# Kernel optimization log

Measured on AMD Instinct MI355X. Metric: run time of the kernel, lower is better.

The kernel has to match this reference:

```python
import jax, jax.numpy as jnp
import numpy as np

D_MODEL, N_HEADS, D_FFN = 256, 8, 1024
HEAD_DIM = D_MODEL // N_HEADS
BZ, H, W = 2, 56, 56
EPS = 1e-5


def _layer_norm(x, g, b):
    m = jnp.mean(x, axis=-1, keepdims=True)
    v = jnp.mean((x - m) ** 2, axis=-1, keepdims=True)
    return (x - m) / jnp.sqrt(v + EPS) * g + b


def _forward(src, posemb_row, posemb_col,
             w_q_row, b_q_row, w_q_col, b_q_col,
             w_k_row, b_k_row, w_k_col, b_k_col,
             w_v, b_v, w_out, b_out,
             norm1_g, norm1_b, lin1_w, lin1_b, lin2_w, lin2_b,
             norm2_g, norm2_b, padding_mask):
    bz, c, h, w = src.shape
    nq = h * w
    x = src.transpose(0, 2, 3, 1)                      # (b,h,w,c)
    x_pr = x + posemb_row[:, None, :, :]               # row posemb broadcast over h
    x_pc = x + posemb_col[:, :, None, :]               # col posemb broadcast over w
    scaling = HEAD_DIM ** -0.5

    q_row = (x_pr.reshape(bz, nq, c) @ w_q_row.T + b_q_row) * scaling
    q_col = (x_pc.reshape(bz, nq, c) @ w_q_col.T + b_q_col) * scaling
    k_row = (x_pr @ w_k_row.T + b_k_row).mean(axis=1)  # (b,w,c): pool over rows
    k_col = (x_pc @ w_k_col.T + b_k_col).mean(axis=2)  # (b,h,c): pool over cols
    v = x @ w_v.T + b_v                                # (b,h,w,c)

    q_row = q_row.reshape(bz, nq, N_HEADS, HEAD_DIM)
    q_col = q_col.reshape(bz, nq, N_HEADS, HEAD_DIM)
    k_row = k_row.reshape(bz, w, N_HEADS, HEAD_DIM)
    k_col = k_col.reshape(bz, h, N_HEADS, HEAD_DIM)
    v = v.reshape(bz, h, w, N_HEADS, HEAD_DIM)

    aw_row = jnp.einsum('bqnd,bwnd->bnqw', q_row, k_row)
    aw_col = jnp.einsum('bqnd,bhnd->bnqh', q_col, k_col)
    neg = jnp.finfo(aw_row.dtype).min
    aw_row = jnp.where(padding_mask[:, 0, :][:, None, None, :], neg, aw_row)
    aw_col = jnp.where(padding_mask[:, :, 0][:, None, None, :], neg, aw_col)
    aw_row = jax.nn.softmax(aw_row, axis=-1)
    aw_col = jax.nn.softmax(aw_col, axis=-1)

    # out[q] = sum_h A_col[q,h] * (sum_w A_row[q,w] * V[h,w])  (RCDA recombination)
    tmp = jnp.einsum('bnqw,bhwnd->bnqhd', aw_row, v)   # dominant intermediate
    attn = jnp.einsum('bnqh,bnqhd->bqnd', aw_col, tmp).reshape(bz, nq, c)
    attn = attn @ w_out.T + b_out                      # (b,hw,c)

    x = _layer_norm(x + attn.reshape(bz, h, w, c), norm1_g, norm1_b)
    y = jax.nn.relu(x @ lin1_w.T + lin1_b) @ lin2_w.T + lin2_b
    x = _layer_norm(x + y, norm2_g, norm2_b)
    return x.transpose(0, 3, 1, 2)                     # (b,c,h,w)


def setup_inputs() -> dict:
    key = jax.random.key(0)
    ks = jax.random.split(key, 12)

    def wmat(k, shape, scale=0.02):
        return jax.random.normal(k, shape, jnp.float32) * scale

    return {
        'src': jax.random.normal(ks[0], (BZ, D_MODEL, H, W), jnp.float32),
        'padding_mask': jnp.zeros((BZ, H, W), jnp.bool_),
        'posemb_row': jax.random.normal(ks[1], (BZ, W, D_MODEL), jnp.float32),
        'posemb_col': jax.random.normal(ks[2], (BZ, H, D_MODEL), jnp.float32),
        'w_q_row': wmat(ks[3], (D_MODEL, D_MODEL)),
        'b_q_row': jnp.zeros((D_MODEL,), jnp.float32),
        'w_q_col': wmat(ks[4], (D_MODEL, D_MODEL)),
        'b_q_col': jnp.zeros((D_MODEL,), jnp.float32),
        'w_k_row': wmat(ks[5], (D_MODEL, D_MODEL)),
        'b_k_row': jnp.zeros((D_MODEL,), jnp.float32),
        'w_k_col': wmat(ks[6], (D_MODEL, D_MODEL)),
        'b_k_col': jnp.zeros((D_MODEL,), jnp.float32),
        'w_v': wmat(ks[7], (D_MODEL, D_MODEL)),
        'b_v': jnp.zeros((D_MODEL,), jnp.float32),
        'w_out': wmat(ks[8], (D_MODEL, D_MODEL)),
        'b_out': jnp.zeros((D_MODEL,), jnp.float32),
        'norm1_g': jnp.ones((D_MODEL,), jnp.float32),
        'norm1_b': jnp.zeros((D_MODEL,), jnp.float32),
        'lin1_w': wmat(ks[9], (D_FFN, D_MODEL)),
        'lin1_b': jnp.zeros((D_FFN,), jnp.float32),
        'lin2_w': wmat(ks[10], (D_MODEL, D_FFN)),
        'lin2_b': jnp.zeros((D_MODEL,), jnp.float32),
        'norm2_g': jnp.ones((D_MODEL,), jnp.float32),
        'norm2_b': jnp.zeros((D_MODEL,), jnp.float32),
    }


def reference(src, padding_mask, posemb_row, posemb_col,
              w_q_row, b_q_row, w_q_col, b_q_col,
              w_k_row, b_k_row, w_k_col, b_k_col,
              w_v, b_v, w_out, b_out,
              norm1_g, norm1_b, lin1_w, lin1_b, lin2_w, lin2_b,
              norm2_g, norm2_b):
    return _forward(src, posemb_row, posemb_col,
                    w_q_row, b_q_row, w_q_col, b_q_col,
                    w_k_row, b_k_row, w_k_col, b_k_col,
                    w_v, b_v, w_out, b_out,
                    norm1_g, norm1_b, lin1_w, lin1_b, lin2_w, lin2_b,
                    norm2_g, norm2_b, padding_mask)
```

## Files before the change

### kernel.cpp

```cpp
#include <hip/hip_runtime.h>
#include <math.h>

#define EPSV 1e-5f
#define SCALV 0.17677669529663687f

typedef __attribute__((ext_vector_type(8))) short s16x8;
typedef __attribute__((ext_vector_type(8))) __bf16 bf8_t;
typedef __attribute__((ext_vector_type(4))) float f32x4;

__device__ inline unsigned short f2bfu(float f) {
  union { float f; unsigned u; } v; v.f = f;
  return (unsigned short)((v.u + 0x7FFFu + ((v.u >> 16) & 1u)) >> 16);
}

__device__ inline f32x4 mfma16(s16x8 a, s16x8 b, f32x4 c) {
  return __builtin_amdgcn_mfma_f32_16x16x32_bf16(
      __builtin_bit_cast(bf8_t, a), __builtin_bit_cast(bf8_t, b), c, 0, 0, 0);
}

__device__ inline void gll16(const void* g, const void* l) {
  __builtin_amdgcn_global_load_lds(
      (const __attribute__((address_space(1))) unsigned*)g,
      (__attribute__((address_space(3))) unsigned*)l, 16, 0, 0);
}

__global__ __launch_bounds__(256) void k_transpose(const float* __restrict__ src,
                                                   float* __restrict__ X,
                                                   short* __restrict__ Xb) {
  __shared__ float tile[32][33];
  int b = blockIdx.z;
  int hw0 = blockIdx.x * 32, c0 = blockIdx.y * 32;
  int tx = threadIdx.x, ty = threadIdx.y;
  for (int i = ty; i < 32; i += 8)
    tile[i][tx] = src[((size_t)(b * 256 + c0 + i)) * 3136 + hw0 + tx];
  __syncthreads();
  for (int i = ty; i < 32; i += 8) {
    float v = tile[tx][i];
    size_t idx = ((size_t)(b * 3136 + hw0 + i)) * 256 + c0 + tx;
    X[idx] = v;
    Xb[idx] = (short)f2bfu(v);
  }
}

__global__ void k_means(const float* __restrict__ src, float* __restrict__ MH, float* __restrict__ MW) {
  int c = blockIdx.x, b = blockIdx.y, t = threadIdx.x;
  if (t >= 56) return;
  const float* p = src + ((size_t)(b * 256 + c)) * 3136;
  float sH = 0.f, sW = 0.f;
  for (int i = 0; i < 56; ++i) {
    sH += p[i * 56 + t];
    sW += p[t * 56 + i];
  }
  MH[((size_t)(b * 56 + t)) * 256 + c] = sH * (1.f / 56.f);
  MW[((size_t)(b * 56 + t)) * 256 + c] = sW * (1.f / 56.f);
}

__global__ __launch_bounds__(256) void k_smallproj(
    const float* __restrict__ per, const float* __restrict__ pec,
    const float* __restrict__ mh, const float* __restrict__ mw,
    const float* __restrict__ wqr, const float* __restrict__ wqc,
    const float* __restrict__ wkr, const float* __restrict__ wkc,
    const float* __restrict__ bkr, const float* __restrict__ bkc,
    float* __restrict__ PRW, float* __restrict__ PCW,
    float* __restrict__ KR, float* __restrict__ KC) {
  __shared__ __align__(16) float inb[256];
  int s = blockIdx.x / 112;
  int r = blockIdx.x % 112;
  int j = threadIdx.x;
  const float* i0; const float* i1 = nullptr; const float* W;
  const float* bias = nullptr; float* out;
  if (s == 0)      { i0 = per; W = wqr; out = PRW; }
  else if (s == 1) { i0 = pec; W = wqc; out = PCW; }
  else if (s == 2) { i0 = per; i1 = mh; W = wkr; bias = bkr; out = KR; }
  else             { i0 = pec; i1 = mw; W = wkc; bias = bkc; out = KC; }
  float v = i0[(size_t)r * 256 + j];
  if (i1) v += i1[(size_t)r * 256 + j];
  inb[j] = v;
  __syncthreads();
  const float* wrow = W + (size_t)j * 256;
  float acc = 0.f;
  #pragma unroll
  for (int c4 = 0; c4 < 64; ++c4) {
    float4 iv = *(const float4*)(&inb[c4 * 4]);
    float4 wv = *(const float4*)(wrow + c4 * 4);
    acc += iv.x * wv.x + iv.y * wv.y + iv.z * wv.z + iv.w * wv.w;
  }
  if (bias) acc += bias[j];
  out[(size_t)r * 256 + j] = acc;
}

__global__ __launch_bounds__(256) void k_pack(
    const float* __restrict__ wqr, const float* __restrict__ wqc, const float* __restrict__ wv,
    const float* __restrict__ wo, const float* __restrict__ l1w, const float* __restrict__ l2w,
    short* __restrict__ Wcat, short* __restrict__ wob,
    short* __restrict__ l1b, short* __restrict__ l2b) {
  int seg = blockIdx.y;
  int e = (blockIdx.x * 256 + threadIdx.x) * 4;
  int cnt = (seg == 0) ? 196608 : (seg == 1) ? 65536 : 262144;
  if (e >= cnt) return;
  const float* sp;
  short* dp;
  if (seg == 0) {
    dp = Wcat + e;
    sp = (e < 65536) ? wqr + e : (e < 131072) ? wqc + (e - 65536) : wv + (e - 131072);
  } else if (seg == 1) { dp = wob + e; sp = wo + e; }
  else if (seg == 2)   { dp = l1b + e; sp = l1w + e; }
  else                 { dp = l2b + e; sp = l2w + e; }
  float4 v = *(const float4*)sp;
  uint2 p;
  p.x = (unsigned)f2bfu(v.x) | ((unsigned)f2bfu(v.y) << 16);
  p.y = (unsigned)f2bfu(v.z) | ((unsigned)f2bfu(v.w) << 16);
  *(uint2*)dp = p;
}

#define GEMM64_CORE(Aptr, Wptr, Kdim)                                           \
  __shared__ __align__(16) short Ls[2][2][4096];                                \
  int tid = threadIdx.x;                                                        \
  int wid = tid >> 6, lane = tid & 63;                                          \
  int ln15 = lane & 15, slot = lane >> 4;                                       \
  int m0 = blockIdx.x * 64, n0 = blockIdx.y * 64;                               \
  int l8 = lane >> 3, c8 = lane & 7;                                            \
  int csw = ((c8 ^ l8) << 4);                                                   \
  int K2 = (Kdim) * 2;                                                          \
  const char* Ag = (const char*)(Aptr) + (size_t)(m0 + wid * 16 + l8) * K2 + csw; \
  const char* Wg = (const char*)(Wptr) + (size_t)(n0 + wid * 16 + l8) * K2 + csw; \
  int u0 = __builtin_amdgcn_readfirstlane(wid * 2048);                          \
  int wm0 = (wid >> 1) << 5, wn0 = (wid & 1) << 5;                              \
  int xr = ln15 & 7;                                                            \
  f32x4 acc[2][2] = {};                                                         \
  int nt = (Kdim) >> 6;                                                         \
  {                                                                             \
    char* bA = (char*)&Ls[0][0][0];                                             \
    char* bB = (char*)&Ls[0][1][0];                                             \
    gll16(Ag, bA + u0);                                                         \
    gll16(Ag + (size_t)8 * K2, bA + u0 + 1024);                                 \
    gll16(Wg, bB + u0);                                                         \
    gll16(Wg + (size_t)8 * K2, bB + u0 + 1024);                                 \
  }                                                                             \
  __syncthreads();                                                              \
  for (int t = 0; t < nt; ++t) {                                                \
    int bf = t & 1;                                                             \
    if (t + 1 < nt) {                                                           \
      size_t ko = (size_t)(t + 1) * 128;                                        \
      char* bA = (char*)&Ls[bf ^ 1][0][0];                                      \
      char* bB = (char*)&Ls[bf ^ 1][1][0];                                      \
      gll16(Ag + ko, bA + u0);                                                  \
      gll16(Ag + ko + (size_t)8 * K2, bA + u0 + 1024);                          \
      gll16(Wg + ko, bB + u0);                                                  \
      gll16(Wg + ko + (size_t)8 * K2, bB + u0 + 1024);                          \
    }                                                                           \
    const char* LA = (const char*)&Ls[bf][0][0];                                \
    const char* LB = (const char*)&Ls[bf][1][0];                                \
    _Pragma("unroll")                                                           \
    for (int kc = 0; kc < 2; ++kc) {                                            \
      s16x8 af[2], bv2[2];                                                      \
      _Pragma("unroll")                                                         \
      for (int mf = 0; mf < 2; ++mf)                                            \
        af[mf] = *(const s16x8*)(LA + (wm0 + mf * 16 + ln15) * 128              \
                                  + (((kc * 4 + slot) ^ xr) << 4));             \
      _Pragma("unroll")                                                         \
      for (int nf = 0; nf < 2; ++nf)                                            \
        bv2[nf] = *(const s16x8*)(LB + (wn0 + nf * 16 + ln15) * 128             \
                                   + (((kc * 4 + slot) ^ xr) << 4));            \
      _Pragma("unroll")                                                         \
      for (int mf = 0; mf < 2; ++mf)                                            \
        _Pragma("unroll")                                                       \
        for (int nf = 0; nf < 2; ++nf)                                          \
          acc[mf][nf] = mfma16(af[mf], bv2[nf], acc[mf][nf]);                   \
    }                                                                           \
    __syncthreads();                                                            \
  }

template<int EPI>
__global__ __launch_bounds__(256) void k_gemm64p(
    const short* __restrict__ A, const short* __restrict__ W,
    const float* __restrict__ bias, float* __restrict__ outF,
    short* __restrict__ outB, int K, int N) {
  GEMM64_CORE(A, W, K)
  #pragma unroll
  for (int mf = 0; mf < 2; ++mf)
    #pragma unroll
    for (int nf = 0; nf < 2; ++nf) {
      int gc = n0 + wn0 + (nf << 4) + ln15;
      float bs = bias[gc];
      #pragma unroll
      for (int r = 0; r < 4; ++r) {
        int gr = m0 + wm0 + (mf << 4) + (slot << 2) + r;
        float v = acc[mf][nf][r] + bs;
        if (EPI == 0) outF[(size_t)gr * N + gc] = v;
        else          outB[(size_t)gr * N + gc] = (short)f2bfu(fmaxf(v, 0.f));
      }
    }
}

__global__ __launch_bounds__(256) void k_proj64p(
    const short* __restrict__ A, const short* __restrict__ W,
    const float* __restrict__ bqr, const float* __restrict__ bqc, const float* __restrict__ bv,
    const float* __restrict__ PRW, const float* __restrict__ PCW,
    float* __restrict__ QR, float* __restrict__ QC, short* __restrict__ Vt) {
  GEMM64_CORE(A, W, 256)
  int s = n0 >> 8;
  #pragma unroll
  for (int mf = 0; mf < 2; ++mf)
    #pragma unroll
    for (int nf = 0; nf < 2; ++nf) {
      f32x4 c = acc[mf][nf];
      int gc = n0 + wn0 + (nf << 4) + ln15;
      int jl = gc & 255;
      #pragma unroll
      for (int r = 0; r < 4; ++r) {
        int gr = m0 + wm0 + (mf << 4) + (slot << 2) + r;
        int bb = gr >= 3136;
        int q = gr - bb * 3136;
        if (s == 0) {
          int w = q % 56;
          QR[(size_t)gr * 256 + jl] =
              (c[r] + PRW[((size_t)(bb * 56 + w)) * 256 + jl] + bqr[jl]) * SCALV;
        } else if (s == 1) {
          int h = q / 56;
          QC[(size_t)gr * 256 + jl] =
              (c[r] + PCW[((size_t)(bb * 56 + h)) * 256 + jl] + bqc[jl]) * SCALV;
        } else {
          int nn = jl >> 5, d = jl & 31;
          int h = q / 56, w = q - h * 56;
          Vt[((size_t)((bb * 8 + nn) * 32 + d)) * 3584 + h * 64 + w] =
              (short)f2bfu(c[r] + bv[jl]);
        }
      }
    }
}

__global__ __launch_bounds__(256) void k_scores2(
    const float* __restrict__ QR, const float* __restrict__ QC,
    const float* __restrict__ KR, const float* __restrict__ KC,
    const unsigned char* __restrict__ pm,
    float* __restrict__ AWR, float* __restrict__ AWC) {
  __shared__ float Ks[56][33];
  int tid = threadIdx.x;
  int n = blockIdx.y & 7;
  int isCol = blockIdx.y >> 3;
  int b = blockIdx.z;
  const float* Kg = isCol ? KC : KR;
  for (int l = tid; l < 56 * 32; l += 256) {
    int w = l >> 5, d = l & 31;
    Ks[w][d] = Kg[((size_t)(b * 56 + w) << 8) + (n << 5) + d];
  }
  __syncthreads();
  int wave = tid >> 6, ln = tid & 63;
  const float* Qbase = (isCol ? QC : QR);
  float* AW = isCol ? AWC : AWR;
  bool msk = (ln < 56) && (isCol ? (pm[(size_t)b * 3136 + ln * 56] != 0)
                                 : (pm[(size_t)b * 3136 + ln] != 0));
  for (int it = 0; it < 8; ++it) {
    int q = blockIdx.x * 32 + wave * 8 + it;
    const float* Qg = Qbase + ((size_t)(b * 3136 + q) << 8) + (n << 5);
    float sc = -INFINITY;
    if (ln < 56) {
      float s = 0.f;
      #pragma unroll
      for (int d4 = 0; d4 < 8; ++d4) {
        float4 qv = *(const float4*)(Qg + d4 * 4);
        s += qv.x * Ks[ln][d4 * 4 + 0] + qv.y * Ks[ln][d4 * 4 + 1]
           + qv.z * Ks[ln][d4 * 4 + 2] + qv.w * Ks[ln][d4 * 4 + 3];
      }
      if (msk) s = -3.402823466e38f;
      sc = s;
    }
    float mx = sc;
    for (int o = 32; o; o >>= 1) mx = fmaxf(mx, __shfl_xor(mx, o));
    float e = (ln < 56) ? __expf(sc - mx) : 0.f;
    float ss = e;
    for (int o = 32; o; o >>= 1) ss += __shfl_xor(ss, o);
    float aw = e / ss;
    if (ln < 56)
      AW[((size_t)(b * 8 + n) * 3136 + q) * 56 + ln] = aw;
  }
}

__global__ __launch_bounds__(256, 4) void k_attn2(
    const float* __restrict__ AWR, const float* __restrict__ AWC,
    const short* __restrict__ Vt, short* __restrict__ ATTb) {
  __shared__ __align__(16) short Vs[4 * 2304];
  __shared__ __align__(16) short Acs[128 * 57];
  int tid = threadIdx.x;
  int wid = tid >> 6, lane = tid & 63;
  int ln15 = lane & 15, slot = lane >> 4;
  int q0 = blockIdx.x * 128;
  int n = blockIdx.y, b = blockIdx.z;
  int bn = b * 8 + n;
  size_t awbase = (size_t)bn * 3136 * 56;
  for (int l = tid; l < 128 * 56; l += 256) {
    int q = l / 56, h = l - (l / 56) * 56;
    int qc = q0 + q; if (qc > 3135) qc = 3135;
    Acs[q * 57 + h] = (short)f2bfu(AWC[awbase + (size_t)qc * 56 + h]);
  }
  s16x8 bfr[2][2];
  #pragma unroll
  for (int qf = 0; qf < 2; ++qf) {
    int qc = q0 + wid * 32 + qf * 16 + ln15; if (qc > 3135) qc = 3135;
    const float* arp = AWR + awbase + (size_t)qc * 56;
    #pragma unroll
    for (int kc = 0; kc < 2; ++kc) {
      if (kc == 1 && slot == 3) {
        s16x8 z = {};
        bfr[qf][1] = z;
      } else {
        float4 t0 = *(const float4*)(arp + kc * 32 + slot * 8);
        float4 t1 = *(const float4*)(arp + kc * 32 + slot * 8 + 4);
        s16x8 f;
        f[0] = (short)f2bfu(t0.x); f[1] = (short)f2bfu(t0.y);
        f[2] = (short)f2bfu(t0.z); f[3] = (short)f2bfu(t0.w);
        f[4] = (short)f2bfu(t1.x); f[5] = (short)f2bfu(t1.y);
        f[6] = (short)f2bfu(t1.z); f[7] = (short)f2bfu(t1.w);
        bfr[qf][kc] = f;
      }
    }
  }
  const short* Vg = Vt + (size_t)bn * 32 * 3584;
  int sd = (tid >> 3) & 31, swp = tid & 7;
  const short* vsrc = Vg + (size_t)sd * 3584 + swp * 8;
  short* vdst = Vs + sd * 72 + swp * 8;
  s16x8 pre[4];
  #pragma unroll
  for (int i = 0; i < 4; ++i)
    pre[i] = *(const s16x8*)(vsrc + (size_t)i * 64);
  #pragma unroll
  for (int i = 0; i < 4; ++i)
    *(s16x8*)(vdst + i * 2304) = pre[i];
  __syncthreads();

  f32x4 oacc[2][2] = {};
  for (int hc = 0; hc < 14; ++hc) {
    if (hc < 13) {
      #pragma unroll
      for (int i = 0; i < 4; ++i)
        pre[i] = *(const s16x8*)(vsrc + (size_t)((hc + 1) * 4 + i) * 64);
    }
    #pragma unroll
    for (int hh = 0; hh < 4; ++hh) {
      int h = hc * 4 + hh;
      s16x8 af[2][2];
      #pragma unroll
      for (int df = 0; df < 2; ++df)
        #pragma unroll
        for (int kc = 0; kc < 2; ++kc)
          af[df][kc] = *(const s16x8*)(Vs + hh * 2304 + (df * 16 + ln15) * 72 + kc * 32 + slot * 8);
      #pragma unroll
      for (int qf = 0; qf < 2; ++qf) {
        float acv = __uint_as_float(
            ((unsigned)(unsigned short)Acs[(wid * 32 + qf * 16 + ln15) * 57 + h]) << 16);
        #pragma unroll
        for (int df = 0; df < 2; ++df) {
          f32x4 tmp = {0.f, 0.f, 0.f, 0.f};
          tmp = mfma16(af[df][0], bfr[qf][0], tmp);
          tmp = mfma16(af[df][1], bfr[qf][1], tmp);
          oacc[df][qf][0] += acv * tmp[0];
          oacc[df][qf][1] += acv * tmp[1];
          oacc[df][qf][2] += acv * tmp[2];
          oacc[df][qf][3] += acv * tmp[3];
        }
      }
    }
    if (hc < 13) {
      __syncthreads();
      #pragma unroll
      for (int i = 0; i < 4; ++i)
        *(s16x8*)(vdst + i * 2304) = pre[i];
      __syncthreads();
    }
  }
  __syncthreads();
  #pragma unroll
  for (int df = 0; df < 2; ++df)
    #pragma unroll
    for (int qf = 0; qf < 2; ++qf) {
      int qi = wid * 32 + qf * 16 + ln15;
      short4 pk;
      pk.x = (short)f2bfu(oacc[df][qf][0]);
      pk.y = (short)f2bfu(oacc[df][qf][1]);
      pk.z = (short)f2bfu(oacc[df][qf][2]);
      pk.w = (short)f2bfu(oacc[df][qf][3]);
      *(short4*)(Vs + qi * 36 + df * 16 + slot * 4) = pk;
    }
  __syncthreads();
  int q = tid >> 1, half = tid & 1;
  int qg = q0 + q;
  if (qg < 3136) {
    s16x8 v = *(const s16x8*)(Vs + q * 36 + half * 16);
    *(s16x8*)(ATTb + ((size_t)(b * 3136 + qg)) * 256 + n * 32 + half * 16) = v;
  }
}

__global__ __launch_bounds__(256) void k_ln1(
    const float* __restrict__ Y, const float* __restrict__ X,
    const float* __restrict__ g, const float* __restrict__ bb,
    float* __restrict__ XN1f, short* __restrict__ XN1b) {
  int tid = threadIdx.x;
  int row = blockIdx.x * 4 + (tid >> 6);
  int ln = tid & 63;
  size_t base = (size_t)row * 256 + ln * 4;
  float4 y = *(const float4*)(Y + base);
  float4 x = *(const float4*)(X + base);
  float v0 = y.x + x.x, v1 = y.y + x.y, v2 = y.z + x.z, v3 = y.w + x.w;
  float s = v0 + v1 + v2 + v3;
  float s2 = v0 * v0 + v1 * v1 + v2 * v2 + v3 * v3;
  for (int o = 32; o; o >>= 1) { s += __shfl_xor(s, o); s2 += __shfl_xor(s2, o); }
  float m = s * (1.f / 256.f);
  float inv = rsqrtf(fmaxf(s2 * (1.f / 256.f) - m * m, 0.f) + EPSV);
  float4 gg = *(const float4*)(g + ln * 4);
  float4 bv = *(const float4*)(bb + ln * 4);
  float4 o4;
  o4.x = (v0 - m) * inv * gg.x + bv.x;
  o4.y = (v1 - m) * inv * gg.y + bv.y;
  o4.z = (v2 - m) * inv * gg.z + bv.z;
  o4.w = (v3 - m) * inv * gg.w + bv.w;
  *(float4*)(XN1f + base) = o4;
  uint2 pk;
  pk.x = (unsigned)f2bfu(o4.x) | ((unsigned)f2bfu(o4.y) << 16);
  pk.y = (unsigned)f2bfu(o4.z) | ((unsigned)f2bfu(o4.w) << 16);
  *(uint2*)(XN1b + base) = pk;
}

__global__ __launch_bounds__(256) void k_ln2t(
    const float* __restrict__ Y2, const float* __restrict__ XN1,
    const float* __restrict__ g, const float* __restrict__ bb,
    float* __restrict__ out) {
  __shared__ float VL[16][257];
  int tid = threadIdx.x;
  int r0 = blockIdx.x * 16;
  for (int l = tid; l < 16 * 256; l += 256) {
    int r = l >> 8, c = l & 255;
    VL[r][c] = Y2[(size_t)(r0 + r) * 256 + c] + XN1[(size_t)(r0 + r) * 256 + c];
  }
  __syncthreads();
  int wv = tid >> 6, ln = tid & 63;
  for (int rr = wv; rr < 16; rr += 4) {
    float s = 0.f, s2 = 0.f;
    float vv[4];
    #pragma unroll
    for (int i = 0; i < 4; ++i) {
      float v = VL[rr][ln * 4 + i];
      vv[i] = v; s += v; s2 += v * v;
    }
    for (int o = 32; o; o >>= 1) { s += __shfl_xor(s, o); s2 += __shfl_xor(s2, o); }
    float m = s * (1.f / 256.f);
    float inv = rsqrtf(fmaxf(s2 * (1.f / 256.f) - m * m, 0.f) + EPSV);
    #pragma unroll
    for (int i = 0; i < 4; ++i) {
      int c = ln * 4 + i;
      VL[rr][c] = (vv[i] - m) * inv * g[c] + bb[c];
    }
  }
  __syncthreads();
  int b = r0 / 3136;
  int hw0 = r0 % 3136;
  int r = tid & 15, cg = tid >> 4;
  for (int it = 0; it < 16; ++it) {
    int c = it * 16 + cg;
    out[(size_t)(b * 256 + c) * 3136 + hw0 + r] = VL[r][c];
  }
}

extern "C" void kernel_launch(void* const* d_in, const int* in_sizes, int n_in,
                              void* d_out, int out_size, void* d_ws, size_t ws_size,
                              hipStream_t stream) {
  const float* src = (const float*)d_in[0];
  const unsigned char* pmask = (const unsigned char*)d_in[1];
  const float* per = (const float*)d_in[2];
  const float* pec = (const float*)d_in[3];
  const float* wqr = (const float*)d_in[4];
  const float* bqr = (const float*)d_in[5];
  const float* wqc = (const float*)d_in[6];
  const float* bqc = (const float*)d_in[7];
  const float* wkr = (const float*)d_in[8];
  const float* bkr = (const float*)d_in[9];
  const float* wkc = (const float*)d_in[10];
  const float* bkc = (const float*)d_in[11];
  const float* wv  = (const float*)d_in[12];
  const float* bv  = (const float*)d_in[13];
  const float* wo  = (const float*)d_in[14];
  const float* bo  = (const float*)d_in[15];
  const float* n1g = (const float*)d_in[16];
  const float* n1b = (const float*)d_in[17];
  const float* l1w = (const float*)d_in[18];
  const float* l1b = (const float*)d_in[19];
  const float* l2w = (const float*)d_in[20];
  const float* l2b = (const float*)d_in[21];
  const float* n2g = (const float*)d_in[22];
  const float* n2b = (const float*)d_in[23];

  float* ws = (float*)d_ws;
  float* X    = ws + 0;
  short* Xb   = (short*)(ws + 1605632);
  float* QR   = ws + 2408448;
  float* QC   = ws + 4014080;
  short* Vt   = (short*)(ws + 5619712);
  float* AWR  = ws + 6537216;
  float* AWC  = ws + 9347072;
  short* ATTb = (short*)(ws + 12156928);
  short* FFb  = (short*)(ws + 12959744);
  float* Y    = ws + 16171008;
  float* XN1f = ws + 17776640;
  short* XN1b = (short*)(ws + 19382272);
  float* MH   = ws + 20185088;
  float* MW   = ws + 20213760;
  float* PRW  = ws + 20242432;
  float* PCW  = ws + 20271104;
  float* KR   = ws + 20299776;
  float* KC   = ws + 20328448;
  short* Wcat = (short*)(ws + 20357120);
  short* wob  = (short*)(ws + 20455424);
  short* l1wb = (short*)(ws + 20488192);
  short* l2wb = (short*)(ws + 20619264);
  float* out = (float*)d_out;

  k_pack<<<dim3(256, 4), 256, 0, stream>>>(wqr, wqc, wv, wo, l1w, l2w,
                                           Wcat, wob, l1wb, l2wb);
  k_transpose<<<dim3(98, 8, 2), dim3(32, 8), 0, stream>>>(src, X, Xb);
  k_means<<<dim3(256, 2), 64, 0, stream>>>(src, MH, MW);
  k_smallproj<<<448, 256, 0, stream>>>(per, pec, MH, MW, wqr, wqc, wkr, wkc,
                                       bkr, bkc, PRW, PCW, KR, KC);
  k_proj64p<<<dim3(98, 12), 256, 0, stream>>>(Xb, Wcat, bqr, bqc, bv,
                                              PRW, PCW, QR, QC, Vt);
  k_scores2<<<dim3(98, 16, 2), 256, 0, stream>>>(QR, QC, KR, KC, pmask, AWR, AWC);
  k_attn2<<<dim3(25, 8, 2), 256, 0, stream>>>(AWR, AWC, Vt, ATTb);
  k_gemm64p<0><<<dim3(98, 4), 256, 0, stream>>>(ATTb, wob, bo, Y, nullptr, 256, 256);
  k_ln1<<<1568, 256, 0, stream>>>(Y, X, n1g, n1b, XN1f, XN1b);
  k_gemm64p<1><<<dim3(98, 16), 256, 0, stream>>>(XN1b, l1wb, l1b, nullptr, FFb, 256, 1024);
  k_gemm64p<0><<<dim3(98, 4), 256, 0, stream>>>(FFb, l2wb, l2b, Y, nullptr, 1024, 256);
  k_ln2t<<<392, 256, 0, stream>>>(Y, XN1f, n2g, n2b, out);
}
```

Before: 255.8 us.

## Fuse score softmax into attention kernel and merge prep kernels

Attention score computation and softmax for both row and column axes now run inside the attention kernel. Their bf16 weights go straight to shared memory, so the full fp32 AWR/AWC matrices are no longer written to or read back from global memory. Transpose and weight packing merge into one launch, and the pooled means are computed from the transposed X inside the small projection kernel, removing two launches. In exchange, the fused kernel runs only 400 blocks that each do serial per-query softmax work, so parallelism drops, and its shared-memory footprint grows.

```diff
diff --git a/kernel.cpp b/kernel.cpp
--- a/kernel.cpp
+++ b/kernel.cpp
@@ -24,40 +24,56 @@
       (__attribute__((address_space(3))) unsigned*)l, 16, 0, 0);
 }
 
-__global__ __launch_bounds__(256) void k_transpose(const float* __restrict__ src,
-                                                   float* __restrict__ X,
-                                                   short* __restrict__ Xb) {
+__global__ __launch_bounds__(256) void k_prep0(
+    const float* __restrict__ src,
+    const float* __restrict__ wqr, const float* __restrict__ wqc, const float* __restrict__ wv,
+    const float* __restrict__ wo, const float* __restrict__ l1w, const float* __restrict__ l2w,
+    float* __restrict__ X, short* __restrict__ Xb,
+    short* __restrict__ Wcat, short* __restrict__ wob,
+    short* __restrict__ l1b, short* __restrict__ l2b) {
   __shared__ float tile[32][33];
-  int b = blockIdx.z;
-  int hw0 = blockIdx.x * 32, c0 = blockIdx.y * 32;
-  int tx = threadIdx.x, ty = threadIdx.y;
-  for (int i = ty; i < 32; i += 8)
-    tile[i][tx] = src[((size_t)(b * 256 + c0 + i)) * 3136 + hw0 + tx];
-  __syncthreads();
-  for (int i = ty; i < 32; i += 8) {
-    float v = tile[tx][i];
-    size_t idx = ((size_t)(b * 3136 + hw0 + i)) * 256 + c0 + tx;
-    X[idx] = v;
-    Xb[idx] = (short)f2bfu(v);
-  }
-}
-
-__global__ void k_means(const float* __restrict__ src, float* __restrict__ MH, float* __restrict__ MW) {
-  int c = blockIdx.x, b = blockIdx.y, t = threadIdx.x;
-  if (t >= 56) return;
-  const float* p = src + ((size_t)(b * 256 + c)) * 3136;
-  float sH = 0.f, sW = 0.f;
-  for (int i = 0; i < 56; ++i) {
-    sH += p[i * 56 + t];
-    sW += p[t * 56 + i];
-  }
-  MH[((size_t)(b * 56 + t)) * 256 + c] = sH * (1.f / 56.f);
-  MW[((size_t)(b * 56 + t)) * 256 + c] = sW * (1.f / 56.f);
-}
-
-__global__ __launch_bounds__(256) void k_smallproj(
+  int bid = blockIdx.x;
+  int tid = threadIdx.x;
+  if (bid < 1568) {
+    int b = bid / 784;
+    int rem = bid - b * 784;
+    int cb = rem / 98, hwb = rem % 98;
+    int hw0 = hwb * 32, c0 = cb * 32;
+    int tx = tid & 31, ty = tid >> 5;
+    for (int i = ty; i < 32; i += 8)
+      tile[i][tx] = src[((size_t)(b * 256 + c0 + i)) * 3136 + hw0 + tx];
+    __syncthreads();
+    for (int i = ty; i < 32; i += 8) {
+      float v = tile[tx][i];
+      size_t idx = ((size_t)(b * 3136 + hw0 + i)) * 256 + c0 + tx;
+      X[idx] = v;
+      Xb[idx] = (short)f2bfu(v);
+    }
+  } else {
+    int pb = bid - 1568;
+    int seg = pb >> 8;
+    int e = (((pb & 255) * 256) + tid) * 4;
+    int cnt = (seg == 0) ? 196608 : (seg == 1) ? 65536 : 262144;
+    if (e >= cnt) return;
+    const float* sp;
+    short* dp;
+    if (seg == 0) {
+      dp = Wcat + e;
+      sp = (e < 65536) ? wqr + e : (e < 131072) ? wqc + (e - 65536) : wv + (e - 131072);
+    } else if (seg == 1) { dp = wob + e; sp = wo + e; }
+    else if (seg == 2)   { dp = l1b + e; sp = l1w + e; }
+    else                 { dp = l2b + e; sp = l2w + e; }
+    float4 v = *(const float4*)sp;
+    uint2 p;
+    p.x = (unsigned)f2bfu(v.x) | ((unsigned)f2bfu(v.y) << 16);
+    p.y = (unsigned)f2bfu(v.z) | ((unsigned)f2bfu(v.w) << 16);
+    *(uint2*)dp = p;
+  }
+}
+
+__global__ __launch_bounds__(256) void k_smallproj2(
     const float* __restrict__ per, const float* __restrict__ pec,
-    const float* __restrict__ mh, const float* __restrict__ mw,
+    const float* __restrict__ X,
     const float* __restrict__ wqr, const float* __restrict__ wqc,
     const float* __restrict__ wkr, const float* __restrict__ wkc,
     const float* __restrict__ bkr, const float* __restrict__ bkc,
@@ -67,14 +83,29 @@
   int s = blockIdx.x / 112;
   int r = blockIdx.x % 112;
   int j = threadIdx.x;
-  const float* i0; const float* i1 = nullptr; const float* W;
-  const float* bias = nullptr; float* out;
-  if (s == 0)      { i0 = per; W = wqr; out = PRW; }
-  else if (s == 1) { i0 = pec; W = wqc; out = PCW; }
-  else if (s == 2) { i0 = per; i1 = mh; W = wkr; bias = bkr; out = KR; }
-  else             { i0 = pec; i1 = mw; W = wkc; bias = bkc; out = KC; }
-  float v = i0[(size_t)r * 256 + j];
-  if (i1) v += i1[(size_t)r * 256 + j];
+  const float* W;
+  const float* bias = nullptr;
+  float* out;
+  float v;
+  if (s == 0) {
+    v = per[(size_t)r * 256 + j]; W = wqr; out = PRW;
+  } else if (s == 1) {
+    v = pec[(size_t)r * 256 + j]; W = wqc; out = PCW;
+  } else if (s == 2) {
+    int b = r / 56, w = r % 56;
+    float sum = 0.f;
+    for (int h = 0; h < 56; ++h)
+      sum += X[((size_t)(b * 3136 + h * 56 + w)) * 256 + j];
+    v = per[(size_t)r * 256 + j] + sum * (1.f / 56.f);
+    W = wkr; bias = bkr; out = KR;
+  } else {
+    int b = r / 56, h = r % 56;
+    float sum = 0.f;
+    for (int w = 0; w < 56; ++w)
+      sum += X[((size_t)(b * 3136 + h * 56 + w)) * 256 + j];
+    v = pec[(size_t)r * 256 + j] + sum * (1.f / 56.f);
+    W = wkc; bias = bkc; out = KC;
+  }
   inb[j] = v;
   __syncthreads();
   const float* wrow = W + (size_t)j * 256;
@@ -87,30 +118,6 @@
   }
   if (bias) acc += bias[j];
   out[(size_t)r * 256 + j] = acc;
-}
-
-__global__ __launch_bounds__(256) void k_pack(
-    const float* __restrict__ wqr, const float* __restrict__ wqc, const float* __restrict__ wv,
-    const float* __restrict__ wo, const float* __restrict__ l1w, const float* __restrict__ l2w,
-    short* __restrict__ Wcat, short* __restrict__ wob,
-    short* __restrict__ l1b, short* __restrict__ l2b) {
-  int seg = blockIdx.y;
-  int e = (blockIdx.x * 256 + threadIdx.x) * 4;
-  int cnt = (seg == 0) ? 196608 : (seg == 1) ? 65536 : 262144;
-  if (e >= cnt) return;
-  const float* sp;
-  short* dp;
-  if (seg == 0) {
-    dp = Wcat + e;
-    sp = (e < 65536) ? wqr + e : (e < 131072) ? wqc + (e - 65536) : wv + (e - 131072);
-  } else if (seg == 1) { dp = wob + e; sp = wo + e; }
-  else if (seg == 2)   { dp = l1b + e; sp = l1w + e; }
-  else                 { dp = l2b + e; sp = l2w + e; }
-  float4 v = *(const float4*)sp;
-  uint2 p;
-  p.x = (unsigned)f2bfu(v.x) | ((unsigned)f2bfu(v.y) << 16);
-  p.y = (unsigned)f2bfu(v.z) | ((unsigned)f2bfu(v.w) << 16);
-  *(uint2*)dp = p;
 }
 
 #define GEMM64_CORE(Aptr, Wptr, Kdim)                                           \
@@ -230,103 +237,102 @@
     }
 }
 
-__global__ __launch_bounds__(256) void k_scores2(
+__global__ __launch_bounds__(256, 2) void k_fattn(
     const float* __restrict__ QR, const float* __restrict__ QC,
     const float* __restrict__ KR, const float* __restrict__ KC,
     const unsigned char* __restrict__ pm,
-    float* __restrict__ AWR, float* __restrict__ AWC) {
-  __shared__ float Ks[56][33];
-  int tid = threadIdx.x;
-  int n = blockIdx.y & 7;
-  int isCol = blockIdx.y >> 3;
-  int b = blockIdx.z;
-  const float* Kg = isCol ? KC : KR;
-  for (int l = tid; l < 56 * 32; l += 256) {
-    int w = l >> 5, d = l & 31;
-    Ks[w][d] = Kg[((size_t)(b * 56 + w) << 8) + (n << 5) + d];
-  }
-  __syncthreads();
-  int wave = tid >> 6, ln = tid & 63;
-  const float* Qbase = (isCol ? QC : QR);
-  float* AW = isCol ? AWC : AWR;
-  bool msk = (ln < 56) && (isCol ? (pm[(size_t)b * 3136 + ln * 56] != 0)
-                                 : (pm[(size_t)b * 3136 + ln] != 0));
-  for (int it = 0; it < 8; ++it) {
-    int q = blockIdx.x * 32 + wave * 8 + it;
-    const float* Qg = Qbase + ((size_t)(b * 3136 + q) << 8) + (n << 5);
-    float sc = -INFINITY;
-    if (ln < 56) {
-      float s = 0.f;
-      #pragma unroll
-      for (int d4 = 0; d4 < 8; ++d4) {
-        float4 qv = *(const float4*)(Qg + d4 * 4);
-        s += qv.x * Ks[ln][d4 * 4 + 0] + qv.y * Ks[ln][d4 * 4 + 1]
-           + qv.z * Ks[ln][d4 * 4 + 2] + qv.w * Ks[ln][d4 * 4 + 3];
-      }
-      if (msk) s = -3.402823466e38f;
-      sc = s;
-    }
-    float mx = sc;
-    for (int o = 32; o; o >>= 1) mx = fmaxf(mx, __shfl_xor(mx, o));
-    float e = (ln < 56) ? __expf(sc - mx) : 0.f;
-    float ss = e;
-    for (int o = 32; o; o >>= 1) ss += __shfl_xor(ss, o);
-    float aw = e / ss;
-    if (ln < 56)
-      AW[((size_t)(b * 8 + n) * 3136 + q) * 56 + ln] = aw;
-  }
-}
-
-__global__ __launch_bounds__(256, 4) void k_attn2(
-    const float* __restrict__ AWR, const float* __restrict__ AWC,
     const short* __restrict__ Vt, short* __restrict__ ATTb) {
-  __shared__ __align__(16) short Vs[4 * 2304];
-  __shared__ __align__(16) short Acs[128 * 57];
+  __shared__ __align__(16) float KsR[56][33];
+  __shared__ __align__(16) float KsC[56][33];
+  __shared__ __align__(16) short Ar[128 * 72];
+  __shared__ __align__(16) short Acs[128 * 56];
+  __shared__ __align__(16) short Vs[4 * 2176];
   int tid = threadIdx.x;
   int wid = tid >> 6, lane = tid & 63;
   int ln15 = lane & 15, slot = lane >> 4;
   int q0 = blockIdx.x * 128;
   int n = blockIdx.y, b = blockIdx.z;
   int bn = b * 8 + n;
-  size_t awbase = (size_t)bn * 3136 * 56;
-  for (int l = tid; l < 128 * 56; l += 256) {
-    int q = l / 56, h = l - (l / 56) * 56;
-    int qc = q0 + q; if (qc > 3135) qc = 3135;
-    Acs[q * 57 + h] = (short)f2bfu(AWC[awbase + (size_t)qc * 56 + h]);
-  }
+  for (int l = tid; l < 56 * 32; l += 256) {
+    int w = l >> 5, d = l & 31;
+    KsR[w][d] = KR[((size_t)(b * 56 + w) << 8) + (n << 5) + d];
+    KsC[w][d] = KC[((size_t)(b * 56 + w) << 8) + (n << 5) + d];
+  }
+  __syncthreads();
+  bool mrow = (lane < 56) && (pm[(size_t)b * 3136 + lane] != 0);
+  bool mcol = (lane < 56) && (pm[(size_t)b * 3136 + lane * 56] != 0);
+  for (int i = 0; i < 32; ++i) {
+    int ql = wid * 32 + i;
+    int q = q0 + ql; if (q > 3135) q = 3135;
+    size_t qoff = ((size_t)(b * 3136 + q) << 8) + (n << 5);
+    {
+      const float* Qg = QR + qoff;
+      float sc = -INFINITY;
+      if (lane < 56) {
+        float s = 0.f;
+        #pragma unroll
+        for (int d4 = 0; d4 < 8; ++d4) {
+          float4 qv = *(const float4*)(Qg + d4 * 4);
+          s += qv.x * KsR[lane][d4 * 4 + 0] + qv.y * KsR[lane][d4 * 4 + 1]
+             + qv.z * KsR[lane][d4 * 4 + 2] + qv.w * KsR[lane][d4 * 4 + 3];
+        }
+        if (mrow) s = -3.402823466e38f;
+        sc = s;
+      }
+      float mx = sc;
+      for (int o = 32; o; o >>= 1) mx = fmaxf(mx, __shfl_xor(mx, o));
+      float e = (lane < 56) ? __expf(sc - mx) : 0.f;
+      float ss = e;
+      for (int o = 32; o; o >>= 1) ss += __shfl_xor(ss, o);
+      if (lane < 56) {
+        Ar[ql * 72 + lane] = (short)f2bfu(e / ss);
+      } else {
+        Ar[ql * 72 + lane] = 0;
+        Ar[ql * 72 + lane + 8] = 0;
+      }
+    }
+    {
+      const float* Qg = QC + qoff;
+      float sc = -INFINITY;
+      if (lane < 56) {
+        float s = 0.f;
+        #pragma unroll
+        for (int d4 = 0; d4 < 8; ++d4) {
+          float4 qv = *(const float4*)(Qg + d4 * 4);
+          s += qv.x * KsC[lane][d4 * 4 + 0] + qv.y * KsC[lane][d4 * 4 + 1]
+             + qv.z * KsC[lane][d4 * 4 + 2] + qv.w * KsC[lane][d4 * 4 + 3];
+        }
+        if (mcol) s = -3.402823466e38f;
+        sc = s;
+      }
+      float mx = sc;
+      for (int o = 32; o; o >>= 1) mx = fmaxf(mx, __shfl_xor(mx, o));
+      float e = (lane < 56) ? __expf(sc - mx) : 0.f;
+      float ss = e;
+      for (int o = 32; o; o >>= 1) ss += __shfl_xor(ss, o);
+      if (lane < 56)
+        Acs[ql * 56 + lane] = (short)f2bfu(e / ss);
+    }
+  }
+  __syncthreads();
   s16x8 bfr[2][2];
   #pragma unroll
-  for (int qf = 0; qf < 2; ++qf) {
-    int qc = q0 + wid * 32 + qf * 16 + ln15; if (qc > 3135) qc = 3135;
-    const float* arp = AWR + awbase + (size_t)qc * 56;
-    #pragma unroll
-    for (int kc = 0; kc < 2; ++kc) {
-      if (kc == 1 && slot == 3) {
-        s16x8 z = {};
-        bfr[qf][1] = z;
-      } else {
-        float4 t0 = *(const float4*)(arp + kc * 32 + slot * 8);
-        float4 t1 = *(const float4*)(arp + kc * 32 + slot * 8 + 4);
-        s16x8 f;
-        f[0] = (short)f2bfu(t0.x); f[1] = (short)f2bfu(t0.y);
-        f[2] = (short)f2bfu(t0.z); f[3] = (short)f2bfu(t0.w);
-        f[4] = (short)f2bfu(t1.x); f[5] = (short)f2bfu(t1.y);
-        f[6] = (short)f2bfu(t1.z); f[7] = (short)f2bfu(t1.w);
-        bfr[qf][kc] = f;
-      }
-    }
-  }
+  for (int qf = 0; qf < 2; ++qf)
+    #pragma unroll
+    for (int kc = 0; kc < 2; ++kc)
+      bfr[qf][kc] = *(const s16x8*)(Ar + (wid * 32 + qf * 16 + ln15) * 72
+                                       + kc * 32 + slot * 8);
   const short* Vg = Vt + (size_t)bn * 32 * 3584;
   int sd = (tid >> 3) & 31, swp = tid & 7;
   const short* vsrc = Vg + (size_t)sd * 3584 + swp * 8;
-  short* vdst = Vs + sd * 72 + swp * 8;
+  short* vdst = Vs + sd * 68 + swp * 8;
   s16x8 pre[4];
   #pragma unroll
   for (int i = 0; i < 4; ++i)
     pre[i] = *(const s16x8*)(vsrc + (size_t)i * 64);
   #pragma unroll
   for (int i = 0; i < 4; ++i)
-    *(s16x8*)(vdst + i * 2304) = pre[i];
+    *(s16x8*)(vdst + i * 2176) = pre[i];
   __syncthreads();
 
   f32x4 oacc[2][2] = {};
@@ -344,11 +350,12 @@
       for (int df = 0; df < 2; ++df)
         #pragma unroll
         for (int kc = 0; kc < 2; ++kc)
-          af[df][kc] = *(const s16x8*)(Vs + hh * 2304 + (df * 16 + ln15) * 72 + kc * 32 + slot * 8);
+          af[df][kc] = *(const s16x8*)(Vs + hh * 2176 + (df * 16 + ln15) * 68
+                                          + kc * 32 + slot * 8);
       #pragma unroll
       for (int qf = 0; qf < 2; ++qf) {
         float acv = __uint_as_float(
-            ((unsigned)(unsigned short)Acs[(wid * 32 + qf * 16 + ln15) * 57 + h]) << 16);
+            ((unsigned)(unsigned short)Acs[(wid * 32 + qf * 16 + ln15) * 56 + h]) << 16);
         #pragma unroll
         for (int df = 0; df < 2; ++df) {
           f32x4 tmp = {0.f, 0.f, 0.f, 0.f};
@@ -365,7 +372,7 @@
       __syncthreads();
       #pragma unroll
       for (int i = 0; i < 4; ++i)
-        *(s16x8*)(vdst + i * 2304) = pre[i];
+        *(s16x8*)(vdst + i * 2176) = pre[i];
       __syncthreads();
     }
   }
@@ -380,13 +387,13 @@
       pk.y = (short)f2bfu(oacc[df][qf][1]);
       pk.z = (short)f2bfu(oacc[df][qf][2]);
       pk.w = (short)f2bfu(oacc[df][qf][3]);
-      *(short4*)(Vs + qi * 36 + df * 16 + slot * 4) = pk;
+      *(short4*)(Ar + qi * 36 + df * 16 + slot * 4) = pk;
     }
   __syncthreads();
   int q = tid >> 1, half = tid & 1;
   int qg = q0 + q;
   if (qg < 3136) {
-    s16x8 v = *(const s16x8*)(Vs + q * 36 + half * 16);
+    s16x8 v = *(const s16x8*)(Ar + q * 36 + half * 16);
     *(s16x8*)(ATTb + ((size_t)(b * 3136 + qg)) * 256 + n * 32 + half * 16) = v;
   }
 }
@@ -495,15 +502,11 @@
   float* QR   = ws + 2408448;
   float* QC   = ws + 4014080;
   short* Vt   = (short*)(ws + 5619712);
-  float* AWR  = ws + 6537216;
-  float* AWC  = ws + 9347072;
   short* ATTb = (short*)(ws + 12156928);
   short* FFb  = (short*)(ws + 12959744);
   float* Y    = ws + 16171008;
   float* XN1f = ws + 17776640;
   short* XN1b = (short*)(ws + 19382272);
-  float* MH   = ws + 20185088;
-  float* MW   = ws + 20213760;
   float* PRW  = ws + 20242432;
   float* PCW  = ws + 20271104;
   float* KR   = ws + 20299776;
@@ -514,16 +517,13 @@
   short* l2wb = (short*)(ws + 20619264);
   float* out = (float*)d_out;
 
-  k_pack<<<dim3(256, 4), 256, 0, stream>>>(wqr, wqc, wv, wo, l1w, l2w,
-                                           Wcat, wob, l1wb, l2wb);
-  k_transpose<<<dim3(98, 8, 2), dim3(32, 8), 0, stream>>>(src, X, Xb);
-  k_means<<<dim3(256, 2), 64, 0, stream>>>(src, MH, MW);
-  k_smallproj<<<448, 256, 0, stream>>>(per, pec, MH, MW, wqr, wqc, wkr, wkc,
-                                       bkr, bkc, PRW, PCW, KR, KC);
+  k_prep0<<<2592, 256, 0, stream>>>(src, wqr, wqc, wv, wo, l1w, l2w,
+                                    X, Xb, Wcat, wob, l1wb, l2wb);
+  k_smallproj2<<<448, 256, 0, stream>>>(per, pec, X, wqr, wqc, wkr, wkc,
+                                        bkr, bkc, PRW, PCW, KR, KC);
   k_proj64p<<<dim3(98, 12), 256, 0, stream>>>(Xb, Wcat, bqr, bqc, bv,
                                               PRW, PCW, QR, QC, Vt);
-  k_scores2<<<dim3(98, 16, 2), 256, 0, stream>>>(QR, QC, KR, KC, pmask, AWR, AWC);
-  k_attn2<<<dim3(25, 8, 2), 256, 0, stream>>>(AWR, AWC, Vt, ATTb);
+  k_fattn<<<dim3(25, 8, 2), 256, 0, stream>>>(QR, QC, KR, KC, pmask, Vt, ATTb);
   k_gemm64p<0><<<dim3(98, 4), 256, 0, stream>>>(ATTb, wob, bo, Y, nullptr, 256, 256);
   k_ln1<<<1568, 256, 0, stream>>>(Y, X, n1g, n1b, XN1f, XN1b);
   k_gemm64p<1><<<dim3(98, 16), 256, 0, stream>>>(XN1b, l1wb, l1b, nullptr, FFb, 256, 1024);
```

New measurement: 266.5 us. 1.04x slower.
